# Kernel optimization log

Measured on AMD Instinct MI355X. Metric: run time of the kernel, lower is better.

Reference implementation:

```python
import jax, jax.numpy as jnp
import numpy as np

K = 8  # kernel_size
COUT = 512


def setup_inputs() -> dict:
    key = jax.random.key(0)
    k1, k2, k3 = jax.random.split(key, 3)
    B, CIN, L = 8, 512, 2048
    x = jax.random.normal(k1, (B, CIN, L), dtype=jnp.float32)
    # nn.Linear(CIN, COUT*K) weight, scaled like kaiming-uniform-ish init
    W = jax.random.normal(k2, (COUT * K, CIN), dtype=jnp.float32) * (1.0 / np.sqrt(CIN))
    b = jax.random.normal(k3, (COUT,), dtype=jnp.float32)
    return {"x": x, "W": W, "b": b}


def reference(x, W, b):
    # x: (B, Cin, L); W: (Cout*K, Cin) with row layout j = k*Cout + co; b: (Cout,)
    B, Cin, L = x.shape
    # pointwise linear expand: (B, Cout*K, L)
    z = jnp.einsum('bcl,oc->bol', x, W)
    z = z.reshape(B, K, COUT, L)  # k-major channel layout
    # causal overlap-add fold: y[b,co,t] = sum_k z[b,k,co,t-k]
    y = z[:, 0]
    for k in range(1, K):  # small fixed kernel-size loop
        y = y.at[:, :, k:].add(z[:, k, :, : L - k])
    return y + b[None, :, None]
```

## Files before the change

kernel.cpp:

```cpp
#include <hip/hip_runtime.h>
#include <hip/hip_bf16.h>
#include <cstdint>
#include <cstddef>

#define CIN   512
#define COUT  512
#define LLEN  2048
#define BATCH 8
#define KTAP  8
#define LPAD  (LLEN + 8)

typedef __bf16 bf16x8_t __attribute__((ext_vector_type(8)));
typedef float  f32x4_t  __attribute__((ext_vector_type(4)));
typedef unsigned short u16x8_t __attribute__((ext_vector_type(8)));

__device__ __forceinline__ unsigned short f2bf(float f) {
  __bf16 h = (__bf16)f;
  return __builtin_bit_cast(unsigned short, h);
}

__device__ __forceinline__ void gl2lds16(unsigned short* lds, const unsigned short* g) {
  __builtin_amdgcn_global_load_lds(
      (const __attribute__((address_space(1))) unsigned int*)g,
      (__attribute__((address_space(3))) unsigned int*)lds,
      16, 0, 0);
}

__global__ __launch_bounds__(256) void prepass_kernel(
    const float* __restrict__ x, unsigned short* __restrict__ xtp,
    const float4* __restrict__ W, u16x8_t* __restrict__ Wb) {
  const int bid = blockIdx.x;
  const int t   = threadIdx.x;

  if (bid >= 2048) {
    int idx = (bid - 2048) * 256 + t;
    float4 a = W[idx * 2], b = W[idx * 2 + 1];
    u16x8_t o;
    o[0] = f2bf(a.x); o[1] = f2bf(a.y); o[2] = f2bf(a.z); o[3] = f2bf(a.w);
    o[4] = f2bf(b.x); o[5] = f2bf(b.y); o[6] = f2bf(b.z); o[7] = f2bf(b.w);
    Wb[idx] = o;
    return;
  }

  __shared__ float tile[64][65];
  const int b  = bid >> 8;
  const int c0 = ((bid >> 5) & 7) * 64;
  const int l0 = (bid & 31) * 64;

  if ((bid & 31) == 0 && t < 64) {
    unsigned short* hp = xtp + ((size_t)b * LPAD + (t >> 3)) * CIN + c0 + (t & 7) * 8;
    *(u16x8_t*)hp = (u16x8_t){0, 0, 0, 0, 0, 0, 0, 0};
  }

  {
    const int cr = t >> 2;
    const int lv = (t & 3) * 16;
    const float* src = x + ((size_t)b * CIN + c0 + cr) * LLEN + l0 + lv;
#pragma unroll
    for (int i = 0; i < 4; ++i) {
      float4 v = *(const float4*)(src + 4 * i);
      tile[cr][lv + 4 * i + 0] = v.x;
      tile[cr][lv + 4 * i + 1] = v.y;
      tile[cr][lv + 4 * i + 2] = v.z;
      tile[cr][lv + 4 * i + 3] = v.w;
    }
  }
  __syncthreads();
  {
    const int l    = t >> 2;
    const int cseg = (t & 3) * 16;
    unsigned short ov[16];
#pragma unroll
    for (int u = 0; u < 16; ++u) ov[u] = f2bf(tile[cseg + u][l]);
    unsigned short* dst = xtp + ((size_t)b * LPAD + 8 + l0 + l) * CIN + c0 + cseg;
    *(u16x8_t*)dst       = *(const u16x8_t*)&ov[0];
    *(u16x8_t*)(dst + 8) = *(const u16x8_t*)&ov[8];
  }
}


__global__ __launch_bounds__(512, 4) void conv_gemm_kernel(
    const unsigned short* __restrict__ Wb,
    const unsigned short* __restrict__ xtp,
    const float* __restrict__ bias,
    float* __restrict__ y)
{
  __shared__ __align__(16) unsigned char smem[67584];

  const int t    = threadIdx.x;
  const int lane = t & 63;
  const int wid  = t >> 6;
  const int wm   = wid & 1;
  const int wn   = (wid >> 1) & 1;
  const int hg   = wid >> 2;
  const int l0   = blockIdx.x * 128;
  const int o0   = blockIdx.y * 128;
  const int b    = blockIdx.z;

  const int quad = lane >> 4;
  const int lrow = lane & 15;

  unsigned short* AsBuf = (unsigned short*)smem;
  unsigned short* BsBuf = (unsigned short*)(smem + 32768);

  f32x4_t acc[4][4];
#pragma unroll
  for (int i = 0; i < 4; ++i)
#pragma unroll
    for (int j = 0; j < 4; ++j)
      acc[i][j] = (f32x4_t){0.f, 0.f, 0.f, 0.f};

  const int srow    = t >> 3;
  const int schunk  = (t & 7) ^ (srow & 7);
  const int lds_off = t * 8;

  const unsigned short* xb = xtp + (size_t)b * LPAD * CIN;

  auto stage_A = [&](int kk, int buf) {
    const unsigned short* asrc =
        Wb + (size_t)((kk & 7) * COUT + o0 + srow) * CIN + (kk >> 3) * 64 + schunk * 8;
#pragma unroll
    for (int rd = 0; rd < 2; ++rd)
      gl2lds16(AsBuf + buf * 8192 + lds_off + rd * 4096, asrc + (size_t)rd * 64 * CIN);
  };
  auto stage_B = [&](int ct, int buf) {
    const int c0 = ct * 64;
    const unsigned short* src = xb + (size_t)(l0 + srow) * CIN + c0 + schunk * 8;
#pragma unroll
    for (int rd = 0; rd < 2; ++rd)
      gl2lds16(BsBuf + buf * 8704 + lds_off + rd * 4096, src + (size_t)rd * 64 * CIN);
    if (t < 64) {
      const int r2  = 128 + (t >> 3);
      const int ch2 = (t & 7) ^ (r2 & 7);
      gl2lds16(BsBuf + buf * 8704 + 128 * 64 + t * 8,
               xb + (size_t)(l0 + r2) * CIN + c0 + ch2 * 8);
    }
  };

  stage_B(0, 0);
  stage_A(0, 0);
  __syncthreads();

#pragma unroll 1
  for (int kk = 0; kk < 64; ++kk) {
    const int k  = kk & 7;
    const int ct = kk >> 3;
    if (kk + 1 < 64) stage_A(kk + 1, (kk + 1) & 1);
    if (k == 7 && ct + 1 < 8) stage_B(ct + 1, (ct + 1) & 1);

    const unsigned short* Ac = AsBuf + (kk & 1) * 8192;
    const unsigned short* Bc = BsBuf + (ct & 1) * 8704;
    bf16x8_t af[4], bfr[4];
#pragma unroll
    for (int i = 0; i < 4; ++i) {
      int row  = wm * 64 + i * 16 + lrow;
      int slot = (hg * 4 + quad) ^ (row & 7);
      af[i] = *(const bf16x8_t*)(Ac + row * 64 + slot * 8);
    }
#pragma unroll
    for (int j = 0; j < 4; ++j) {
      int row  = (8 - k) + wn * 64 + j * 16 + lrow;
      int slot = (hg * 4 + quad) ^ (row & 7);
      bfr[j] = *(const bf16x8_t*)(Bc + row * 64 + slot * 8);
    }
    __builtin_amdgcn_s_setprio(1);
#pragma unroll
    for (int i = 0; i < 4; ++i)
#pragma unroll
      for (int j = 0; j < 4; ++j)
        acc[i][j] = __builtin_amdgcn_mfma_f32_16x16x32_bf16(af[i], bfr[j], acc[i][j], 0, 0, 0);
    __builtin_amdgcn_s_setprio(0);
    __syncthreads();
  }

  float* red = (float*)smem + (size_t)(wn * 2 + wm) * 4096;
  if (hg == 1) {
#pragma unroll
    for (int i = 0; i < 4; ++i)
#pragma unroll
      for (int j = 0; j < 4; ++j)
#pragma unroll
        for (int r = 0; r < 4; ++r)
          red[((i * 4 + j) * 4 + r) * 64 + lane] = acc[i][j][r];
  }
  __syncthreads();
  if (hg == 0) {
#pragma unroll
    for (int i = 0; i < 4; ++i) {
      const int o_base = o0 + wm * 64 + i * 16 + quad * 4;
      const float4 bv = *(const float4*)(bias + o_base);
      const float bvr[4] = {bv.x, bv.y, bv.z, bv.w};
#pragma unroll
      for (int j = 0; j < 4; ++j) {
        const int l = l0 + wn * 64 + j * 16 + lrow;
#pragma unroll
        for (int r = 0; r < 4; ++r) {
          float v = acc[i][j][r] + red[((i * 4 + j) * 4 + r) * 64 + lane];
          y[((size_t)b * COUT + o_base + r) * LLEN + l] = v + bvr[r];
        }
      }
    }
  }
}


extern "C" void kernel_launch(void* const* d_in, const int* in_sizes, int n_in,
                              void* d_out, int out_size, void* d_ws, size_t ws_size,
                              hipStream_t stream) {
  const float* x    = (const float*)d_in[0];
  const float* W    = (const float*)d_in[1];
  const float* bias = (const float*)d_in[2];
  float* y          = (float*)d_out;

  unsigned short* xtp = (unsigned short*)d_ws;
  unsigned short* Wb  = (unsigned short*)((char*)d_ws +
                        (size_t)BATCH * LPAD * CIN * sizeof(unsigned short));

  prepass_kernel<<<2048 + 1024, 256, 0, stream>>>(
      x, xtp, (const float4*)W, (u16x8_t*)Wb);
  conv_gemm_kernel<<<dim3(LLEN / 128, COUT / 128, BATCH), 512, 0, stream>>>(
      Wb, xtp, bias, y);
}
```

Measured before the change: 147.8 us.

## Pre-swizzle weights into MFMA fragment order and load A directly to registers

The prepass now writes the bf16 weights in a layout that matches the per-lane MFMA A-fragment order. The GEMM kernel can then load A fragments straight from global memory into registers instead of staging them through LDS. The main loop is restructured to iterate over channel tiles with the 8 taps unrolled inside, so block-wide barriers drop from one per tap-tile to one per channel tile. The trade-off is that global-load latency now sits on the MFMA path without an explicit double-buffered prefetch, and it relies on L2 hits for the weight reuse across blocks.

```diff
diff --git a/kernel.cpp b/kernel.cpp
--- a/kernel.cpp
+++ b/kernel.cpp
@@ -28,7 +28,7 @@
 
 __global__ __launch_bounds__(256) void prepass_kernel(
     const float* __restrict__ x, unsigned short* __restrict__ xtp,
-    const float4* __restrict__ W, u16x8_t* __restrict__ Wb) {
+    const float4* __restrict__ W, u16x8_t* __restrict__ Wf) {
   const int bid = blockIdx.x;
   const int t   = threadIdx.x;
 
@@ -38,7 +38,15 @@
     u16x8_t o;
     o[0] = f2bf(a.x); o[1] = f2bf(a.y); o[2] = f2bf(a.z); o[3] = f2bf(a.w);
     o[4] = f2bf(b.x); o[5] = f2bf(b.y); o[6] = f2bf(b.z); o[7] = f2bf(b.w);
-    Wb[idx] = o;
+    const int row  = idx >> 6;
+    const int cch  = idx & 63;
+    const int k    = row >> 9, oo = row & 511;
+    const int o128 = oo >> 7, wm = (oo >> 6) & 1, fi = (oo >> 4) & 3, lrow = oo & 15;
+    const int ct   = cch >> 3, chin = cch & 7, hg = chin >> 2, quad = chin & 3;
+    const int lane = quad * 16 + lrow;
+    const int off  = k * 32768 + o128 * 8192 + wm * 4096 + hg * 2048 +
+                     ct * 256 + fi * 64 + lane;
+    Wf[off] = o;
     return;
   }
 
@@ -80,12 +88,12 @@
 
 
 __global__ __launch_bounds__(512, 4) void conv_gemm_kernel(
-    const unsigned short* __restrict__ Wb,
+    const unsigned short* __restrict__ Wf,
     const unsigned short* __restrict__ xtp,
     const float* __restrict__ bias,
     float* __restrict__ y)
 {
-  __shared__ __align__(16) unsigned char smem[67584];
+  __shared__ __align__(16) unsigned char smem[65536];
 
   const int t    = threadIdx.x;
   const int lane = t & 63;
@@ -100,8 +108,7 @@
   const int quad = lane >> 4;
   const int lrow = lane & 15;
 
-  unsigned short* AsBuf = (unsigned short*)smem;
-  unsigned short* BsBuf = (unsigned short*)(smem + 32768);
+  unsigned short* BsBuf = (unsigned short*)smem;
 
   f32x4_t acc[4][4];
 #pragma unroll
@@ -116,13 +123,6 @@
 
   const unsigned short* xb = xtp + (size_t)b * LPAD * CIN;
 
-  auto stage_A = [&](int kk, int buf) {
-    const unsigned short* asrc =
-        Wb + (size_t)((kk & 7) * COUT + o0 + srow) * CIN + (kk >> 3) * 64 + schunk * 8;
-#pragma unroll
-    for (int rd = 0; rd < 2; ++rd)
-      gl2lds16(AsBuf + buf * 8192 + lds_off + rd * 4096, asrc + (size_t)rd * 64 * CIN);
-  };
   auto stage_B = [&](int ct, int buf) {
     const int c0 = ct * 64;
     const unsigned short* src = xb + (size_t)(l0 + srow) * CIN + c0 + schunk * 8;
@@ -137,39 +137,37 @@
     }
   };
 
+  const u16x8_t* Wfp = (const u16x8_t*)Wf;
+  const int woff = blockIdx.y * 8192 + wm * 4096 + hg * 2048 + lane;
+
   stage_B(0, 0);
-  stage_A(0, 0);
   __syncthreads();
 
 #pragma unroll 1
-  for (int kk = 0; kk < 64; ++kk) {
-    const int k  = kk & 7;
-    const int ct = kk >> 3;
-    if (kk + 1 < 64) stage_A(kk + 1, (kk + 1) & 1);
-    if (k == 7 && ct + 1 < 8) stage_B(ct + 1, (ct + 1) & 1);
-
-    const unsigned short* Ac = AsBuf + (kk & 1) * 8192;
+  for (int ct = 0; ct < 8; ++ct) {
+    if (ct + 1 < 8) stage_B(ct + 1, (ct + 1) & 1);
     const unsigned short* Bc = BsBuf + (ct & 1) * 8704;
-    bf16x8_t af[4], bfr[4];
-#pragma unroll
-    for (int i = 0; i < 4; ++i) {
-      int row  = wm * 64 + i * 16 + lrow;
-      int slot = (hg * 4 + quad) ^ (row & 7);
-      af[i] = *(const bf16x8_t*)(Ac + row * 64 + slot * 8);
-    }
-#pragma unroll
-    for (int j = 0; j < 4; ++j) {
-      int row  = (8 - k) + wn * 64 + j * 16 + lrow;
-      int slot = (hg * 4 + quad) ^ (row & 7);
-      bfr[j] = *(const bf16x8_t*)(Bc + row * 64 + slot * 8);
-    }
-    __builtin_amdgcn_s_setprio(1);
-#pragma unroll
-    for (int i = 0; i < 4; ++i)
-#pragma unroll
-      for (int j = 0; j < 4; ++j)
-        acc[i][j] = __builtin_amdgcn_mfma_f32_16x16x32_bf16(af[i], bfr[j], acc[i][j], 0, 0, 0);
-    __builtin_amdgcn_s_setprio(0);
+    const u16x8_t* wp = Wfp + woff + ct * 256;
+#pragma unroll
+    for (int k = 0; k < 8; ++k) {
+      bf16x8_t af[4], bfr[4];
+#pragma unroll
+      for (int i = 0; i < 4; ++i)
+        af[i] = __builtin_bit_cast(bf16x8_t, wp[k * 32768 + i * 64]);
+#pragma unroll
+      for (int j = 0; j < 4; ++j) {
+        int row  = (8 - k) + wn * 64 + j * 16 + lrow;
+        int slot = (hg * 4 + quad) ^ (row & 7);
+        bfr[j] = *(const bf16x8_t*)(Bc + row * 64 + slot * 8);
+      }
+      __builtin_amdgcn_s_setprio(1);
+#pragma unroll
+      for (int i = 0; i < 4; ++i)
+#pragma unroll
+        for (int j = 0; j < 4; ++j)
+          acc[i][j] = __builtin_amdgcn_mfma_f32_16x16x32_bf16(af[i], bfr[j], acc[i][j], 0, 0, 0);
+      __builtin_amdgcn_s_setprio(0);
+    }
     __syncthreads();
   }
 
@@ -213,11 +211,11 @@
   float* y          = (float*)d_out;
 
   unsigned short* xtp = (unsigned short*)d_ws;
-  unsigned short* Wb  = (unsigned short*)((char*)d_ws +
+  unsigned short* Wf  = (unsigned short*)((char*)d_ws +
                         (size_t)BATCH * LPAD * CIN * sizeof(unsigned short));
 
   prepass_kernel<<<2048 + 1024, 256, 0, stream>>>(
-      x, xtp, (const float4*)W, (u16x8_t*)Wb);
+      x, xtp, (const float4*)W, (u16x8_t*)Wf);
   conv_gemm_kernel<<<dim3(LLEN / 128, COUT / 128, BATCH), 512, 0, stream>>>(
-      Wb, xtp, bias, y);
-}
+      Wf, xtp, bias, y);
+}
```

After: 144.8 us. 1.02x faster.
